# Kernel tuning notes

Hardware: AMD Instinct MI355X
Metric: run time of the kernel (lower is better)

The kernel has to match this reference:

```python
import jax, jax.numpy as jnp
import numpy as np

N = 40000      # nodes
E = 640000     # edges (avg degree 16)
F_IN = 33      # input residue features (hard-coded in module)
H = 128        # hidden_channels
C_OUT = 3      # output classes (hard-coded)
L = 8          # num_layers
ALPHA = 0.1
THETA = 0.5


def setup_inputs() -> dict:
    key = jax.random.key(0)
    ks = jax.random.split(key, 8)
    x = jax.random.normal(ks[0], (N, F_IN), jnp.float32)
    edge_row = jax.random.randint(ks[1], (E,), 0, N)
    edge_col = jax.random.randint(ks[2], (E,), 0, N)
    edge_weight = jax.random.uniform(ks[3], (E,), jnp.float32)
    # nn.Linear stores weight as [out, in]
    W_in = jax.random.normal(ks[4], (H, F_IN), jnp.float32) * 0.1
    b_in = jnp.zeros((H,), jnp.float32)
    W_out = jax.random.normal(ks[5], (C_OUT, H), jnp.float32) * 0.1
    b_out = jnp.zeros((C_OUT,), jnp.float32)
    # GCN2Conv shared weight1 per layer: [L, H, H]
    W_conv = jax.random.normal(ks[6], (L, H, H), jnp.float32) * (1.0 / np.sqrt(H))
    return dict(x=x, edge_row=edge_row, edge_col=edge_col, edge_weight=edge_weight,
                W_in=W_in, b_in=b_in, W_out=W_out, b_out=b_out, W_conv=W_conv)


def reference(x, edge_row, edge_col, edge_weight, W_in, b_in, W_out, b_out, W_conv):
    # dropout p=0.0 -> identity (also eval mode)
    x0 = jax.nn.relu(x @ W_in.T + b_in)                      # [N, H]
    # GCN2Conv beta_l = log(theta / layer + 1), layer = 1..L
    betas = jnp.log(THETA / jnp.arange(1.0, L + 1.0, dtype=jnp.float32) + 1.0)

    def spmm(h):
        # adj_t @ h : gather source-node features, weight, scatter-add to rows
        return jax.ops.segment_sum(edge_weight[:, None] * h[edge_col], edge_row,
                                   num_segments=N)

    def step(xc, lw):
        W, beta = lw
        # GCN2Conv (shared_weights=True, normalize=False):
        #   xx = (1-alpha)*A@h + alpha*x0 ; out = (1-beta)*xx + beta*(xx@W)
        xx = (1.0 - ALPHA) * spmm(xc) + ALPHA * x0
        out = (1.0 - beta) * xx + beta * (xx @ W)
        return xc + jax.nn.relu(out), None                   # residual in GCN.forward

    x_final, _ = jax.lax.scan(step, x0, (W_conv, betas))
    return x_final @ W_out.T + b_out                          # [N, 3]
```

## Files before the change

### kernel.cpp

```cpp
#include <hip/hip_runtime.h>
#include <hip/hip_bf16.h>
#include <math.h>

#define N_NODES 40000
#define NE      640000
#define FIN     33
#define H       128
#define COUT    3
#define NLAYERS 8
#define ALPHA   0.1f
#define THETA   0.5f
#define CAP     96

#define SB_SCAT 625
#define SB_WPRE 512
#define SB_XIN  2500

typedef __bf16 bf16x8 __attribute__((ext_vector_type(8)));
typedef float  f32x4  __attribute__((ext_vector_type(4)));

__device__ inline unsigned short f2bf(float f) {
    __hip_bfloat16 b = __float2bfloat16(f);
    return *(unsigned short*)&b;
}
__device__ inline float bf2f(unsigned short u) {
    __hip_bfloat16 b = *(__hip_bfloat16*)&u;
    return __bfloat162float(b);
}

__global__ __launch_bounds__(256) void k_setup(
        const int* __restrict__ row, const int* __restrict__ col,
        const float* __restrict__ w, int* __restrict__ cnt,
        unsigned int* __restrict__ bucket,
        const float* __restrict__ Wconv, unsigned short* __restrict__ Wtbf,
        const float* __restrict__ x, const float* __restrict__ Win,
        const float* __restrict__ bin,
        unsigned short* __restrict__ x0bf) {
    __shared__ float sW[H * FIN];
    __shared__ float sx[16][FIN];
    int b = blockIdx.x, t = threadIdx.x;

    if (b < SB_SCAT) {
        int e0 = (b * 256 + t) * 4;
        int r[4], pos[4];
        unsigned int rec[4];
        #pragma unroll
        for (int i = 0; i < 4; i++) {
            int e = e0 + i;
            r[i] = row[e];
            unsigned int wb = f2bf((1.0f - ALPHA) * w[e]);
            rec[i] = (wb << 16) | (unsigned int)col[e];
        }
        #pragma unroll
        for (int i = 0; i < 4; i++) pos[i] = atomicAdd(&cnt[r[i]], 1);
        #pragma unroll
        for (int i = 0; i < 4; i++) bucket[(size_t)r[i] * CAP + pos[i]] = rec[i];
        return;
    }
    if (b < SB_SCAT + SB_WPRE) {
        int idx = (b - SB_SCAT) * 256 + t;
        int l = idx >> 14;
        int rem = idx & 16383;
        int k = rem >> 7, j = rem & 127;
        float beta = logf(THETA / (float)(l + 1) + 1.0f);
        float v = beta * Wconv[idx];
        if (j == k) v += 1.0f - beta;
        Wtbf[l * 16384 + j * 128 + k] = f2bf(v);
        return;
    }
    {
        int n0 = (b - SB_SCAT - SB_WPRE) * 16;
        for (int i = t; i < H * FIN; i += 256) sW[i] = Win[i];
        for (int i = t; i < 16 * FIN; i += 256)
            sx[i / FIN][i % FIN] = x[(size_t)(n0 + i / FIN) * FIN + (i % FIN)];
        __syncthreads();
        int f = t % H;
        int l0 = t / H;
        float bv = bin[f];
        for (int lo = l0; lo < 16; lo += 2) {
            float acc = bv;
            #pragma unroll
            for (int k = 0; k < FIN; k++) acc += sx[lo][k] * sW[f * FIN + k];
            acc = fmaxf(acc, 0.f);
            x0bf[(size_t)(n0 + lo) * H + f] = f2bf(acc);
        }
    }
}

__global__ __launch_bounds__(256) void k_layer(
        const int* __restrict__ cnt, const unsigned int* __restrict__ bucket,
        const unsigned short* __restrict__ hin,
        const unsigned short* __restrict__ x0bf,
        const unsigned short* __restrict__ Wt,
        unsigned short* __restrict__ hout,
        const float* __restrict__ Wout, const float* __restrict__ bout,
        float* __restrict__ out, int do_out) {
    __shared__ __align__(16) char smem[16896];

    int t = threadIdx.x;
    int wv = t >> 6, lane = t & 63;
    int rbase = blockIdx.x * 32;

    {
        int slot = lane >> 4;
        int fid  = lane & 15;
        for (int i = 0; i < 8; i++) {
            int rloc = wv * 8 + i;
            int row  = rbase + rloc;
            int deg  = cnt[row];
            const unsigned int* ep = bucket + (size_t)row * CAP;
            float acc[8] = {0,0,0,0,0,0,0,0};

            for (int e = 0; e < deg; e += 16) {
                unsigned int u[4];
                uint4 q[4];
                #pragma unroll
                for (int k = 0; k < 4; k++) {
                    int ei = e + k * 4 + slot;
                    unsigned int uu = ep[ei];
                    u[k] = (ei < deg) ? uu : 0u;
                }
                #pragma unroll
                for (int k = 0; k < 4; k++)
                    q[k] = *(const uint4*)(hin + (size_t)(u[k] & 0xffffu) * H + fid * 8);
                #pragma unroll
                for (int k = 0; k < 4; k++) {
                    float w = bf2f((unsigned short)(u[k] >> 16));
                    acc[0] += w * bf2f((unsigned short)(q[k].x & 0xffffu));
                    acc[1] += w * bf2f((unsigned short)(q[k].x >> 16));
                    acc[2] += w * bf2f((unsigned short)(q[k].y & 0xffffu));
                    acc[3] += w * bf2f((unsigned short)(q[k].y >> 16));
                    acc[4] += w * bf2f((unsigned short)(q[k].z & 0xffffu));
                    acc[5] += w * bf2f((unsigned short)(q[k].z >> 16));
                    acc[6] += w * bf2f((unsigned short)(q[k].w & 0xffffu));
                    acc[7] += w * bf2f((unsigned short)(q[k].w >> 16));
                }
            }
            #pragma unroll
            for (int j = 0; j < 8; j++) {
                acc[j] += __shfl_xor(acc[j], 16);
                acc[j] += __shfl_xor(acc[j], 32);
            }
            if (slot == 0) {
                uint4 xq = *(const uint4*)(x0bf + (size_t)row * H + fid * 8);
                float o0 = acc[0] + ALPHA * bf2f((unsigned short)(xq.x & 0xffffu));
                float o1 = acc[1] + ALPHA * bf2f((unsigned short)(xq.x >> 16));
                float o2 = acc[2] + ALPHA * bf2f((unsigned short)(xq.y & 0xffffu));
                float o3 = acc[3] + ALPHA * bf2f((unsigned short)(xq.y >> 16));
                float o4 = acc[4] + ALPHA * bf2f((unsigned short)(xq.z & 0xffffu));
                float o5 = acc[5] + ALPHA * bf2f((unsigned short)(xq.z >> 16));
                float o6 = acc[6] + ALPHA * bf2f((unsigned short)(xq.w & 0xffffu));
                float o7 = acc[7] + ALPHA * bf2f((unsigned short)(xq.w >> 16));
                uint4 r;
                r.x = (unsigned int)f2bf(o0) | ((unsigned int)f2bf(o1) << 16);
                r.y = (unsigned int)f2bf(o2) | ((unsigned int)f2bf(o3) << 16);
                r.z = (unsigned int)f2bf(o4) | ((unsigned int)f2bf(o5) << 16);
                r.w = (unsigned int)f2bf(o6) | ((unsigned int)f2bf(o7) << 16);
                *(uint4*)(smem + (size_t)rloc * 272 + fid * 16) = r;
            }
        }
    }
    __syncthreads();

    int quad = lane >> 4, l16 = lane & 15;
    int rh = (wv >> 1) * 16;
    int ch = (wv & 1) * 64;
    f32x4 acc2[4];
    #pragma unroll
    for (int j = 0; j < 4; j++) acc2[j] = (f32x4){0.f, 0.f, 0.f, 0.f};

    #pragma unroll
    for (int k0 = 0; k0 < 4; k0++) {
        bf16x8 av = *(const bf16x8*)(smem + (size_t)(rh + l16) * 272 + k0 * 64 + quad * 16);
        #pragma unroll
        for (int j = 0; j < 4; j++) {
            bf16x8 bv = *(const bf16x8*)(Wt + (size_t)(ch + j * 16 + l16) * H + k0 * 32 + quad * 8);
            acc2[j] = __builtin_amdgcn_mfma_f32_16x16x32_bf16(av, bv, acc2[j], 0, 0, 0);
        }
    }
    __syncthreads();

    float* facc = (float*)smem;
    #pragma unroll
    for (int j = 0; j < 4; j++) {
        #pragma unroll
        for (int r = 0; r < 4; r++)
            facc[(rh + quad * 4 + r) * 132 + ch + j * 16 + l16] = acc2[j][r];
    }
    __syncthreads();

    int cb = (t & 15) * 8;
    #pragma unroll
    for (int p = 0; p < 2; p++) {
        int rloc = p * 16 + (t >> 4);
        int row  = rbase + rloc;
        const float* fr = facc + rloc * 132 + cb;
        f32x4 a0 = *(const f32x4*)fr;
        f32x4 a1 = *(const f32x4*)(fr + 4);
        uint4 hq = *(const uint4*)(hin + (size_t)row * H + cb);
        float hv[8];
        hv[0] = bf2f((unsigned short)(hq.x & 0xffffu)) + fmaxf(a0[0], 0.f);
        hv[1] = bf2f((unsigned short)(hq.x >> 16))     + fmaxf(a0[1], 0.f);
        hv[2] = bf2f((unsigned short)(hq.y & 0xffffu)) + fmaxf(a0[2], 0.f);
        hv[3] = bf2f((unsigned short)(hq.y >> 16))     + fmaxf(a0[3], 0.f);
        hv[4] = bf2f((unsigned short)(hq.z & 0xffffu)) + fmaxf(a1[0], 0.f);
        hv[5] = bf2f((unsigned short)(hq.z >> 16))     + fmaxf(a1[1], 0.f);
        hv[6] = bf2f((unsigned short)(hq.w & 0xffffu)) + fmaxf(a1[2], 0.f);
        hv[7] = bf2f((unsigned short)(hq.w >> 16))     + fmaxf(a1[3], 0.f);

        if (!do_out) {
            uint4 rr;
            rr.x = (unsigned int)f2bf(hv[0]) | ((unsigned int)f2bf(hv[1]) << 16);
            rr.y = (unsigned int)f2bf(hv[2]) | ((unsigned int)f2bf(hv[3]) << 16);
            rr.z = (unsigned int)f2bf(hv[4]) | ((unsigned int)f2bf(hv[5]) << 16);
            rr.w = (unsigned int)f2bf(hv[6]) | ((unsigned int)f2bf(hv[7]) << 16);
            *(uint4*)(hout + (size_t)row * H + cb) = rr;
        } else {
            float p0 = 0.f, p1 = 0.f, p2 = 0.f;
            #pragma unroll
            for (int i2 = 0; i2 < 8; i2++) {
                float h = hv[i2];
                p0 += h * Wout[cb + i2];
                p1 += h * Wout[H + cb + i2];
                p2 += h * Wout[2 * H + cb + i2];
            }
            #pragma unroll
            for (int off = 1; off < 16; off <<= 1) {
                p0 += __shfl_xor(p0, off);
                p1 += __shfl_xor(p1, off);
                p2 += __shfl_xor(p2, off);
            }
            if ((t & 15) == 0) {
                out[(size_t)row * 3 + 0] = p0 + bout[0];
                out[(size_t)row * 3 + 1] = p1 + bout[1];
                out[(size_t)row * 3 + 2] = p2 + bout[2];
            }
        }
    }
}

extern "C" void kernel_launch(void* const* d_in, const int* in_sizes, int n_in,
                              void* d_out, int out_size, void* d_ws, size_t ws_size,
                              hipStream_t stream) {
    const float* x     = (const float*)d_in[0];
    const int*   erow  = (const int*)  d_in[1];
    const int*   ecol  = (const int*)  d_in[2];
    const float* ew    = (const float*)d_in[3];
    const float* Win   = (const float*)d_in[4];
    const float* bin   = (const float*)d_in[5];
    const float* Wout  = (const float*)d_in[6];
    const float* bout  = (const float*)d_in[7];
    const float* Wconv = (const float*)d_in[8];
    float* out = (float*)d_out;

    char* ws = (char*)d_ws;
    const size_t NHb = (size_t)N_NODES * H * sizeof(unsigned short);
    unsigned short* x0bf  = (unsigned short*)(ws);
    unsigned short* bufA  = (unsigned short*)(ws + NHb);
    unsigned short* bufB  = (unsigned short*)(ws + 2 * NHb);
    char* p = ws + 3 * NHb;
    unsigned short* Wtbf  = (unsigned short*)p;  p += 8 * H * H * 2;
    int*  cnt     = (int*) p;  p += 160256;
    unsigned int* bucket = (unsigned int*)p;

    hipMemsetAsync(cnt, 0, (size_t)N_NODES * 4, stream);
    k_setup<<<SB_SCAT + SB_WPRE + SB_XIN, 256, 0, stream>>>(
        erow, ecol, ew, cnt, bucket, Wconv, Wtbf, x, Win, bin, x0bf);

    for (int l = 0; l < NLAYERS; l++) {
        const unsigned short* hin = (l == 0) ? x0bf : ((l & 1) ? bufA : bufB);
        unsigned short* hout = (l & 1) ? bufB : bufA;
        k_layer<<<N_NODES / 32, 256, 0, stream>>>(
            cnt, bucket, hin, x0bf, Wtbf + (size_t)l * H * H,
            hout, Wout, bout, out, (l == NLAYERS - 1) ? 1 : 0);
    }
}
```

Baseline: 392.2 us.

## Gather neighbor features as per-row scaled FP8 instead of BF16 in SpMM

Each layer now writes a second copy of the hidden state as FP8 (e4m3) with a per-row max scale, and the sparse aggregation gathers these 128-byte rows plus a scale instead of 256-byte BF16 rows. This halves the random-gather traffic that dominates the SpMM. The residual path keeps a single in-place BF16 buffer. The cost is lower precision in the aggregated features, an extra scale load per edge, a per-row max reduction, and extra FP8 writes per layer.

```diff
diff --git a/kernel.cpp b/kernel.cpp
--- a/kernel.cpp
+++ b/kernel.cpp
@@ -18,6 +18,7 @@
 
 typedef __bf16 bf16x8 __attribute__((ext_vector_type(8)));
 typedef float  f32x4  __attribute__((ext_vector_type(4)));
+typedef float  f32x2  __attribute__((ext_vector_type(2)));
 
 __device__ inline unsigned short f2bf(float f) {
     __hip_bfloat16 b = __float2bfloat16(f);
@@ -35,9 +36,11 @@
         const float* __restrict__ Wconv, unsigned short* __restrict__ Wtbf,
         const float* __restrict__ x, const float* __restrict__ Win,
         const float* __restrict__ bin,
-        unsigned short* __restrict__ x0bf) {
+        unsigned short* __restrict__ x0bf, unsigned char* __restrict__ hf8,
+        float* __restrict__ scl) {
     __shared__ float sW[H * FIN];
     __shared__ float sx[16][FIN];
+    __shared__ int   srm[16];
     int b = blockIdx.x, t = threadIdx.x;
 
     if (b < SB_SCAT) {
@@ -73,26 +76,49 @@
         for (int i = t; i < H * FIN; i += 256) sW[i] = Win[i];
         for (int i = t; i < 16 * FIN; i += 256)
             sx[i / FIN][i % FIN] = x[(size_t)(n0 + i / FIN) * FIN + (i % FIN)];
+        if (t < 16) srm[t] = 0;
         __syncthreads();
         int f = t % H;
         int l0 = t / H;
         float bv = bin[f];
-        for (int lo = l0; lo < 16; lo += 2) {
+        float av[8];
+        #pragma unroll
+        for (int j = 0; j < 8; j++) {
+            int lo = l0 + j * 2;
             float acc = bv;
             #pragma unroll
             for (int k = 0; k < FIN; k++) acc += sx[lo][k] * sW[f * FIN + k];
             acc = fmaxf(acc, 0.f);
+            av[j] = acc;
             x0bf[(size_t)(n0 + lo) * H + f] = f2bf(acc);
+            atomicMax(&srm[lo], __float_as_int(acc));
+        }
+        __syncthreads();
+        #pragma unroll
+        for (int j = 0; j < 8; j++) {
+            int lo = l0 + j * 2;
+            float rm = __int_as_float(srm[lo]);
+            float s448 = rm > 0.f ? 448.f / rm : 0.f;
+            float q  = av[j] * s448;
+            float qn = __shfl_xor(q, 1);
+            if ((f & 1) == 0) {
+                int d = __builtin_amdgcn_cvt_pk_fp8_f32(q, qn, 0, false);
+                *(unsigned short*)(hf8 + (size_t)(n0 + lo) * H + f) =
+                    (unsigned short)(d & 0xffff);
+            }
+            if (f == 0) scl[n0 + lo] = rm * (1.0f / 448.f);
         }
     }
 }
 
 __global__ __launch_bounds__(256) void k_layer(
         const int* __restrict__ cnt, const unsigned int* __restrict__ bucket,
-        const unsigned short* __restrict__ hin,
+        const unsigned char* __restrict__ f8in, const float* __restrict__ scl_in,
+        unsigned char* __restrict__ f8out, float* __restrict__ scl_out,
+        const unsigned short* __restrict__ hres_in,
+        unsigned short* __restrict__ hres_out,
         const unsigned short* __restrict__ x0bf,
         const unsigned short* __restrict__ Wt,
-        unsigned short* __restrict__ hout,
         const float* __restrict__ Wout, const float* __restrict__ bout,
         float* __restrict__ out, int do_out) {
     __shared__ __align__(16) char smem[16896];
@@ -102,61 +128,69 @@
     int rbase = blockIdx.x * 32;
 
     {
-        int slot = lane >> 4;
-        int fid  = lane & 15;
+        int slot = lane >> 3;
+        int fid  = lane & 7;
         for (int i = 0; i < 8; i++) {
             int rloc = wv * 8 + i;
             int row  = rbase + rloc;
             int deg  = cnt[row];
             const unsigned int* ep = bucket + (size_t)row * CAP;
-            float acc[8] = {0,0,0,0,0,0,0,0};
+            float acc[16];
+            #pragma unroll
+            for (int j = 0; j < 16; j++) acc[j] = 0.f;
 
             for (int e = 0; e < deg; e += 16) {
-                unsigned int u[4];
-                uint4 q[4];
-                #pragma unroll
-                for (int k = 0; k < 4; k++) {
-                    int ei = e + k * 4 + slot;
+                unsigned int u[2];
+                float sc[2];
+                uint4 q[2];
+                #pragma unroll
+                for (int k = 0; k < 2; k++) {
+                    int ei = e + k * 8 + slot;
                     unsigned int uu = ep[ei];
                     u[k] = (ei < deg) ? uu : 0u;
                 }
                 #pragma unroll
-                for (int k = 0; k < 4; k++)
-                    q[k] = *(const uint4*)(hin + (size_t)(u[k] & 0xffffu) * H + fid * 8);
-                #pragma unroll
-                for (int k = 0; k < 4; k++) {
-                    float w = bf2f((unsigned short)(u[k] >> 16));
-                    acc[0] += w * bf2f((unsigned short)(q[k].x & 0xffffu));
-                    acc[1] += w * bf2f((unsigned short)(q[k].x >> 16));
-                    acc[2] += w * bf2f((unsigned short)(q[k].y & 0xffffu));
-                    acc[3] += w * bf2f((unsigned short)(q[k].y >> 16));
-                    acc[4] += w * bf2f((unsigned short)(q[k].z & 0xffffu));
-                    acc[5] += w * bf2f((unsigned short)(q[k].z >> 16));
-                    acc[6] += w * bf2f((unsigned short)(q[k].w & 0xffffu));
-                    acc[7] += w * bf2f((unsigned short)(q[k].w >> 16));
+                for (int k = 0; k < 2; k++) sc[k] = scl_in[u[k] & 0xffffu];
+                #pragma unroll
+                for (int k = 0; k < 2; k++)
+                    q[k] = *(const uint4*)(f8in + (size_t)(u[k] & 0xffffu) * H + fid * 16);
+                #pragma unroll
+                for (int k = 0; k < 2; k++) {
+                    float w = bf2f((unsigned short)(u[k] >> 16)) * sc[k];
+                    unsigned int dw[4] = {q[k].x, q[k].y, q[k].z, q[k].w};
+                    #pragma unroll
+                    for (int d = 0; d < 4; d++) {
+                        f32x2 lo = __builtin_amdgcn_cvt_pk_f32_fp8(dw[d], false);
+                        f32x2 hi = __builtin_amdgcn_cvt_pk_f32_fp8(dw[d], true);
+                        acc[d * 4 + 0] += w * lo.x;
+                        acc[d * 4 + 1] += w * lo.y;
+                        acc[d * 4 + 2] += w * hi.x;
+                        acc[d * 4 + 3] += w * hi.y;
+                    }
                 }
             }
             #pragma unroll
-            for (int j = 0; j < 8; j++) {
+            for (int j = 0; j < 16; j++) {
+                acc[j] += __shfl_xor(acc[j], 8);
                 acc[j] += __shfl_xor(acc[j], 16);
                 acc[j] += __shfl_xor(acc[j], 32);
             }
             if (slot == 0) {
-                uint4 xq = *(const uint4*)(x0bf + (size_t)row * H + fid * 8);
-                float o0 = acc[0] + ALPHA * bf2f((unsigned short)(xq.x & 0xffffu));
-                float o1 = acc[1] + ALPHA * bf2f((unsigned short)(xq.x >> 16));
-                float o2 = acc[2] + ALPHA * bf2f((unsigned short)(xq.y & 0xffffu));
-                float o3 = acc[3] + ALPHA * bf2f((unsigned short)(xq.y >> 16));
-                float o4 = acc[4] + ALPHA * bf2f((unsigned short)(xq.z & 0xffffu));
-                float o5 = acc[5] + ALPHA * bf2f((unsigned short)(xq.z >> 16));
-                float o6 = acc[6] + ALPHA * bf2f((unsigned short)(xq.w & 0xffffu));
-                float o7 = acc[7] + ALPHA * bf2f((unsigned short)(xq.w >> 16));
-                uint4 r;
-                r.x = (unsigned int)f2bf(o0) | ((unsigned int)f2bf(o1) << 16);
-                r.y = (unsigned int)f2bf(o2) | ((unsigned int)f2bf(o3) << 16);
-                r.z = (unsigned int)f2bf(o4) | ((unsigned int)f2bf(o5) << 16);
-                r.w = (unsigned int)f2bf(o6) | ((unsigned int)f2bf(o7) << 16);
-                *(uint4*)(smem + (size_t)rloc * 272 + fid * 16) = r;
+                uint4 xa = *(const uint4*)(x0bf + (size_t)row * H + fid * 16);
+                uint4 xb = *(const uint4*)(x0bf + (size_t)row * H + fid * 16 + 8);
+                unsigned int xw[8] = {xa.x, xa.y, xa.z, xa.w, xb.x, xb.y, xb.z, xb.w};
+                uint4 r0, r1;
+                unsigned int rr[8];
+                #pragma unroll
+                for (int p = 0; p < 8; p++) {
+                    float o0 = acc[p * 2 + 0] + ALPHA * bf2f((unsigned short)(xw[p] & 0xffffu));
+                    float o1 = acc[p * 2 + 1] + ALPHA * bf2f((unsigned short)(xw[p] >> 16));
+                    rr[p] = (unsigned int)f2bf(o0) | ((unsigned int)f2bf(o1) << 16);
+                }
+                r0.x = rr[0]; r0.y = rr[1]; r0.z = rr[2]; r0.w = rr[3];
+                r1.x = rr[4]; r1.y = rr[5]; r1.z = rr[6]; r1.w = rr[7];
+                *(uint4*)(smem + (size_t)rloc * 272 + fid * 32) = r0;
+                *(uint4*)(smem + (size_t)rloc * 272 + fid * 32 + 16) = r1;
             }
         }
     }
@@ -197,7 +231,7 @@
         const float* fr = facc + rloc * 132 + cb;
         f32x4 a0 = *(const f32x4*)fr;
         f32x4 a1 = *(const f32x4*)(fr + 4);
-        uint4 hq = *(const uint4*)(hin + (size_t)row * H + cb);
+        uint4 hq = *(const uint4*)(hres_in + (size_t)row * H + cb);
         float hv[8];
         hv[0] = bf2f((unsigned short)(hq.x & 0xffffu)) + fmaxf(a0[0], 0.f);
         hv[1] = bf2f((unsigned short)(hq.x >> 16))     + fmaxf(a0[1], 0.f);
@@ -214,7 +248,21 @@
             rr.y = (unsigned int)f2bf(hv[2]) | ((unsigned int)f2bf(hv[3]) << 16);
             rr.z = (unsigned int)f2bf(hv[4]) | ((unsigned int)f2bf(hv[5]) << 16);
             rr.w = (unsigned int)f2bf(hv[6]) | ((unsigned int)f2bf(hv[7]) << 16);
-            *(uint4*)(hout + (size_t)row * H + cb) = rr;
+            *(uint4*)(hres_out + (size_t)row * H + cb) = rr;
+            float rm = hv[0];
+            #pragma unroll
+            for (int j = 1; j < 8; j++) rm = fmaxf(rm, hv[j]);
+            #pragma unroll
+            for (int off = 1; off < 16; off <<= 1)
+                rm = fmaxf(rm, __shfl_xor(rm, off));
+            float s448 = rm > 0.f ? 448.f / rm : 0.f;
+            int d0 = __builtin_amdgcn_cvt_pk_fp8_f32(hv[0] * s448, hv[1] * s448, 0, false);
+            d0     = __builtin_amdgcn_cvt_pk_fp8_f32(hv[2] * s448, hv[3] * s448, d0, true);
+            int d1 = __builtin_amdgcn_cvt_pk_fp8_f32(hv[4] * s448, hv[5] * s448, 0, false);
+            d1     = __builtin_amdgcn_cvt_pk_fp8_f32(hv[6] * s448, hv[7] * s448, d1, true);
+            uint2 f8v; f8v.x = (unsigned int)d0; f8v.y = (unsigned int)d1;
+            *(uint2*)(f8out + (size_t)row * H + cb) = f8v;
+            if ((t & 15) == 0) scl_out[row] = rm * (1.0f / 448.f);
         } else {
             float p0 = 0.f, p1 = 0.f, p2 = 0.f;
             #pragma unroll
@@ -255,23 +303,31 @@
 
     char* ws = (char*)d_ws;
     const size_t NHb = (size_t)N_NODES * H * sizeof(unsigned short);
-    unsigned short* x0bf  = (unsigned short*)(ws);
-    unsigned short* bufA  = (unsigned short*)(ws + NHb);
-    unsigned short* bufB  = (unsigned short*)(ws + 2 * NHb);
-    char* p = ws + 3 * NHb;
-    unsigned short* Wtbf  = (unsigned short*)p;  p += 8 * H * H * 2;
-    int*  cnt     = (int*) p;  p += 160256;
+    const size_t NH8 = (size_t)N_NODES * H;
+    unsigned short* x0bf = (unsigned short*)(ws);
+    unsigned short* hbf  = (unsigned short*)(ws + NHb);
+    unsigned char*  hf8A = (unsigned char*)(ws + 2 * NHb);
+    unsigned char*  hf8B = (unsigned char*)(ws + 2 * NHb + NH8);
+    char* p = ws + 2 * NHb + 2 * NH8;
+    unsigned short* Wtbf = (unsigned short*)p;  p += 8 * H * H * 2;
+    int*   cnt  = (int*)  p;  p += 160256;
+    float* sclA = (float*)p;  p += 160256;
+    float* sclB = (float*)p;  p += 160256;
     unsigned int* bucket = (unsigned int*)p;
 
     hipMemsetAsync(cnt, 0, (size_t)N_NODES * 4, stream);
     k_setup<<<SB_SCAT + SB_WPRE + SB_XIN, 256, 0, stream>>>(
-        erow, ecol, ew, cnt, bucket, Wconv, Wtbf, x, Win, bin, x0bf);
+        erow, ecol, ew, cnt, bucket, Wconv, Wtbf, x, Win, bin, x0bf, hf8A, sclA);
 
     for (int l = 0; l < NLAYERS; l++) {
-        const unsigned short* hin = (l == 0) ? x0bf : ((l & 1) ? bufA : bufB);
-        unsigned short* hout = (l & 1) ? bufB : bufA;
+        const unsigned char* f8in  = (l & 1) ? hf8B : hf8A;
+        unsigned char*       f8out = (l & 1) ? hf8A : hf8B;
+        const float* scl_in  = (l & 1) ? sclB : sclA;
+        float*       scl_out = (l & 1) ? sclA : sclB;
+        const unsigned short* hres_in = (l == 0) ? x0bf : hbf;
         k_layer<<<N_NODES / 32, 256, 0, stream>>>(
-            cnt, bucket, hin, x0bf, Wtbf + (size_t)l * H * H,
-            hout, Wout, bout, out, (l == NLAYERS - 1) ? 1 : 0);
-    }
-}
+            cnt, bucket, f8in, scl_in, f8out, scl_out, hres_in, hbf, x0bf,
+            Wtbf + (size_t)l * H * H, Wout, bout, out,
+            (l == NLAYERS - 1) ? 1 : 0);
+    }
+}
```

Result: slower. 456.9 us (+16.5%).

## Gather neighbor features in scaled FP8 instead of BF16 for layers after the first

Applied to the files above, without the earlier changes.

Each layer's output is now also stored as FP8 (e4m3), scaled by a global running max that is tracked with atomicMax. The next layer's sparse aggregation gathers these 1-byte values and dequantizes them with the matching scale. This halves the bytes moved by the random neighbor gathers, which dominate the cost. The residual path keeps a single in-place BF16 buffer. The quantization scale for a layer's output comes from the previous layer's max with a fixed headroom of 16, so values can clip or lose precision, which puts accuracy tolerance at risk.

```diff
diff --git a/kernel.cpp b/kernel.cpp
--- a/kernel.cpp
+++ b/kernel.cpp
@@ -11,6 +11,7 @@
 #define ALPHA   0.1f
 #define THETA   0.5f
 #define CAP     96
+#define HEADROOM 16.0f
 
 #define SB_SCAT 625
 #define SB_WPRE 512
@@ -18,6 +19,7 @@
 
 typedef __bf16 bf16x8 __attribute__((ext_vector_type(8)));
 typedef float  f32x4  __attribute__((ext_vector_type(4)));
+typedef float  f32x2  __attribute__((ext_vector_type(2)));
 
 __device__ inline unsigned short f2bf(float f) {
     __hip_bfloat16 b = __float2bfloat16(f);
@@ -35,7 +37,7 @@
         const float* __restrict__ Wconv, unsigned short* __restrict__ Wtbf,
         const float* __restrict__ x, const float* __restrict__ Win,
         const float* __restrict__ bin,
-        unsigned short* __restrict__ x0bf) {
+        unsigned short* __restrict__ x0bf, int* __restrict__ gmaxb) {
     __shared__ float sW[H * FIN];
     __shared__ float sx[16][FIN];
     int b = blockIdx.x, t = threadIdx.x;
@@ -77,24 +79,28 @@
         int f = t % H;
         int l0 = t / H;
         float bv = bin[f];
+        float tmax = 0.f;
         for (int lo = l0; lo < 16; lo += 2) {
             float acc = bv;
             #pragma unroll
             for (int k = 0; k < FIN; k++) acc += sx[lo][k] * sW[f * FIN + k];
             acc = fmaxf(acc, 0.f);
+            tmax = fmaxf(tmax, acc);
             x0bf[(size_t)(n0 + lo) * H + f] = f2bf(acc);
         }
-    }
-}
-
-__global__ __launch_bounds__(256) void k_layer(
+        #pragma unroll
+        for (int off = 1; off < 64; off <<= 1)
+            tmax = fmaxf(tmax, __shfl_xor(tmax, off));
+        if ((t & 63) == 0) atomicMax(&gmaxb[0], __float_as_int(tmax));
+    }
+}
+
+__global__ __launch_bounds__(256) void k_layer0(
         const int* __restrict__ cnt, const unsigned int* __restrict__ bucket,
-        const unsigned short* __restrict__ hin,
         const unsigned short* __restrict__ x0bf,
         const unsigned short* __restrict__ Wt,
-        unsigned short* __restrict__ hout,
-        const float* __restrict__ Wout, const float* __restrict__ bout,
-        float* __restrict__ out, int do_out) {
+        unsigned short* __restrict__ hbf,
+        unsigned char* __restrict__ f8out, int* __restrict__ gmaxb) {
     __shared__ __align__(16) char smem[16896];
 
     int t = threadIdx.x;
@@ -122,7 +128,7 @@
                 }
                 #pragma unroll
                 for (int k = 0; k < 4; k++)
-                    q[k] = *(const uint4*)(hin + (size_t)(u[k] & 0xffffu) * H + fid * 8);
+                    q[k] = *(const uint4*)(x0bf + (size_t)(u[k] & 0xffffu) * H + fid * 8);
                 #pragma unroll
                 for (int k = 0; k < 4; k++) {
                     float w = bf2f((unsigned short)(u[k] >> 16));
@@ -168,7 +174,6 @@
     f32x4 acc2[4];
     #pragma unroll
     for (int j = 0; j < 4; j++) acc2[j] = (f32x4){0.f, 0.f, 0.f, 0.f};
-
     #pragma unroll
     for (int k0 = 0; k0 < 4; k0++) {
         bf16x8 av = *(const bf16x8*)(smem + (size_t)(rh + l16) * 272 + k0 * 64 + quad * 16);
@@ -189,7 +194,10 @@
     }
     __syncthreads();
 
+    float g0 = __int_as_float(gmaxb[0]);
+    float Q = g0 > 0.f ? 448.f / (HEADROOM * g0) : 0.f;
     int cb = (t & 15) * 8;
+    float rmax = 0.f;
     #pragma unroll
     for (int p = 0; p < 2; p++) {
         int rloc = p * 16 + (t >> 4);
@@ -197,7 +205,7 @@
         const float* fr = facc + rloc * 132 + cb;
         f32x4 a0 = *(const f32x4*)fr;
         f32x4 a1 = *(const f32x4*)(fr + 4);
-        uint4 hq = *(const uint4*)(hin + (size_t)row * H + cb);
+        uint4 hq = *(const uint4*)(x0bf + (size_t)row * H + cb);
         float hv[8];
         hv[0] = bf2f((unsigned short)(hq.x & 0xffffu)) + fmaxf(a0[0], 0.f);
         hv[1] = bf2f((unsigned short)(hq.x >> 16))     + fmaxf(a0[1], 0.f);
@@ -208,13 +216,177 @@
         hv[6] = bf2f((unsigned short)(hq.w & 0xffffu)) + fmaxf(a1[2], 0.f);
         hv[7] = bf2f((unsigned short)(hq.w >> 16))     + fmaxf(a1[3], 0.f);
 
+        uint4 rr;
+        rr.x = (unsigned int)f2bf(hv[0]) | ((unsigned int)f2bf(hv[1]) << 16);
+        rr.y = (unsigned int)f2bf(hv[2]) | ((unsigned int)f2bf(hv[3]) << 16);
+        rr.z = (unsigned int)f2bf(hv[4]) | ((unsigned int)f2bf(hv[5]) << 16);
+        rr.w = (unsigned int)f2bf(hv[6]) | ((unsigned int)f2bf(hv[7]) << 16);
+        *(uint4*)(hbf + (size_t)row * H + cb) = rr;
+
+        int d0 = __builtin_amdgcn_cvt_pk_fp8_f32(hv[0] * Q, hv[1] * Q, 0, false);
+        d0     = __builtin_amdgcn_cvt_pk_fp8_f32(hv[2] * Q, hv[3] * Q, d0, true);
+        int d1 = __builtin_amdgcn_cvt_pk_fp8_f32(hv[4] * Q, hv[5] * Q, 0, false);
+        d1     = __builtin_amdgcn_cvt_pk_fp8_f32(hv[6] * Q, hv[7] * Q, d1, true);
+        uint2 f8v; f8v.x = (unsigned int)d0; f8v.y = (unsigned int)d1;
+        *(uint2*)(f8out + (size_t)row * H + cb) = f8v;
+
+        #pragma unroll
+        for (int j = 0; j < 8; j++) rmax = fmaxf(rmax, hv[j]);
+    }
+    #pragma unroll
+    for (int off = 1; off < 64; off <<= 1)
+        rmax = fmaxf(rmax, __shfl_xor(rmax, off));
+    if ((t & 63) == 0) atomicMax(&gmaxb[1], __float_as_int(rmax));
+}
+
+__global__ __launch_bounds__(256) void k_layerf8(
+        const int* __restrict__ cnt, const unsigned int* __restrict__ bucket,
+        const unsigned char* __restrict__ f8in,
+        unsigned char* __restrict__ f8out,
+        unsigned short* __restrict__ hbf,
+        const unsigned short* __restrict__ x0bf,
+        const unsigned short* __restrict__ Wt,
+        int* __restrict__ gmaxb, int li,
+        const float* __restrict__ Wout, const float* __restrict__ bout,
+        float* __restrict__ out, int do_out) {
+    __shared__ __align__(16) char smem[16896];
+
+    int t = threadIdx.x;
+    int wv = t >> 6, lane = t & 63;
+    int rbase = blockIdx.x * 32;
+
+    float gin = __int_as_float(gmaxb[li - 1]);
+    float D = gin > 0.f ? (HEADROOM / 448.f) * gin : 0.f;
+
+    {
+        int slot = lane >> 3;
+        int fid  = lane & 7;
+        for (int i = 0; i < 8; i++) {
+            int rloc = wv * 8 + i;
+            int row  = rbase + rloc;
+            int deg  = cnt[row];
+            const unsigned int* ep = bucket + (size_t)row * CAP;
+            float acc[16];
+            #pragma unroll
+            for (int j = 0; j < 16; j++) acc[j] = 0.f;
+
+            for (int e = 0; e < deg; e += 16) {
+                unsigned int u[2];
+                uint4 q[2];
+                #pragma unroll
+                for (int k = 0; k < 2; k++) {
+                    int ei = e + k * 8 + slot;
+                    unsigned int uu = ep[ei];
+                    u[k] = (ei < deg) ? uu : 0u;
+                }
+                #pragma unroll
+                for (int k = 0; k < 2; k++)
+                    q[k] = *(const uint4*)(f8in + (size_t)(u[k] & 0xffffu) * H + fid * 16);
+                #pragma unroll
+                for (int k = 0; k < 2; k++) {
+                    float w = bf2f((unsigned short)(u[k] >> 16));
+                    unsigned int dw[4] = {q[k].x, q[k].y, q[k].z, q[k].w};
+                    #pragma unroll
+                    for (int d = 0; d < 4; d++) {
+                        f32x2 lo = __builtin_amdgcn_cvt_pk_f32_fp8(dw[d], false);
+                        f32x2 hi = __builtin_amdgcn_cvt_pk_f32_fp8(dw[d], true);
+                        acc[d * 4 + 0] += w * lo.x;
+                        acc[d * 4 + 1] += w * lo.y;
+                        acc[d * 4 + 2] += w * hi.x;
+                        acc[d * 4 + 3] += w * hi.y;
+                    }
+                }
+            }
+            #pragma unroll
+            for (int j = 0; j < 16; j++) {
+                acc[j] += __shfl_xor(acc[j], 8);
+                acc[j] += __shfl_xor(acc[j], 16);
+                acc[j] += __shfl_xor(acc[j], 32);
+            }
+            if (slot == 0) {
+                uint4 xa = *(const uint4*)(x0bf + (size_t)row * H + fid * 16);
+                uint4 xb = *(const uint4*)(x0bf + (size_t)row * H + fid * 16 + 8);
+                unsigned int xw[8] = {xa.x, xa.y, xa.z, xa.w, xb.x, xb.y, xb.z, xb.w};
+                uint4 r0, r1;
+                unsigned int rr[8];
+                #pragma unroll
+                for (int p = 0; p < 8; p++) {
+                    float o0 = acc[p * 2 + 0] * D + ALPHA * bf2f((unsigned short)(xw[p] & 0xffffu));
+                    float o1 = acc[p * 2 + 1] * D + ALPHA * bf2f((unsigned short)(xw[p] >> 16));
+                    rr[p] = (unsigned int)f2bf(o0) | ((unsigned int)f2bf(o1) << 16);
+                }
+                r0.x = rr[0]; r0.y = rr[1]; r0.z = rr[2]; r0.w = rr[3];
+                r1.x = rr[4]; r1.y = rr[5]; r1.z = rr[6]; r1.w = rr[7];
+                *(uint4*)(smem + (size_t)rloc * 272 + fid * 32) = r0;
+                *(uint4*)(smem + (size_t)rloc * 272 + fid * 32 + 16) = r1;
+            }
+        }
+    }
+    __syncthreads();
+
+    int quad = lane >> 4, l16 = lane & 15;
+    int rh = (wv >> 1) * 16;
+    int ch = (wv & 1) * 64;
+    f32x4 acc2[4];
+    #pragma unroll
+    for (int j = 0; j < 4; j++) acc2[j] = (f32x4){0.f, 0.f, 0.f, 0.f};
+    #pragma unroll
+    for (int k0 = 0; k0 < 4; k0++) {
+        bf16x8 av = *(const bf16x8*)(smem + (size_t)(rh + l16) * 272 + k0 * 64 + quad * 16);
+        #pragma unroll
+        for (int j = 0; j < 4; j++) {
+            bf16x8 bv = *(const bf16x8*)(Wt + (size_t)(ch + j * 16 + l16) * H + k0 * 32 + quad * 8);
+            acc2[j] = __builtin_amdgcn_mfma_f32_16x16x32_bf16(av, bv, acc2[j], 0, 0, 0);
+        }
+    }
+    __syncthreads();
+
+    float* facc = (float*)smem;
+    #pragma unroll
+    for (int j = 0; j < 4; j++) {
+        #pragma unroll
+        for (int r = 0; r < 4; r++)
+            facc[(rh + quad * 4 + r) * 132 + ch + j * 16 + l16] = acc2[j][r];
+    }
+    __syncthreads();
+
+    float gq = __int_as_float(gmaxb[li]);
+    float Q = gq > 0.f ? 448.f / (HEADROOM * gq) : 0.f;
+    int cb = (t & 15) * 8;
+    float rmax = 0.f;
+    #pragma unroll
+    for (int p = 0; p < 2; p++) {
+        int rloc = p * 16 + (t >> 4);
+        int row  = rbase + rloc;
+        const float* fr = facc + rloc * 132 + cb;
+        f32x4 a0 = *(const f32x4*)fr;
+        f32x4 a1 = *(const f32x4*)(fr + 4);
+        uint4 hq = *(const uint4*)(hbf + (size_t)row * H + cb);
+        float hv[8];
+        hv[0] = bf2f((unsigned short)(hq.x & 0xffffu)) + fmaxf(a0[0], 0.f);
+        hv[1] = bf2f((unsigned short)(hq.x >> 16))     + fmaxf(a0[1], 0.f);
+        hv[2] = bf2f((unsigned short)(hq.y & 0xffffu)) + fmaxf(a0[2], 0.f);
+        hv[3] = bf2f((unsigned short)(hq.y >> 16))     + fmaxf(a0[3], 0.f);
+        hv[4] = bf2f((unsigned short)(hq.z & 0xffffu)) + fmaxf(a1[0], 0.f);
+        hv[5] = bf2f((unsigned short)(hq.z >> 16))     + fmaxf(a1[1], 0.f);
+        hv[6] = bf2f((unsigned short)(hq.w & 0xffffu)) + fmaxf(a1[2], 0.f);
+        hv[7] = bf2f((unsigned short)(hq.w >> 16))     + fmaxf(a1[3], 0.f);
+
         if (!do_out) {
             uint4 rr;
             rr.x = (unsigned int)f2bf(hv[0]) | ((unsigned int)f2bf(hv[1]) << 16);
             rr.y = (unsigned int)f2bf(hv[2]) | ((unsigned int)f2bf(hv[3]) << 16);
             rr.z = (unsigned int)f2bf(hv[4]) | ((unsigned int)f2bf(hv[5]) << 16);
             rr.w = (unsigned int)f2bf(hv[6]) | ((unsigned int)f2bf(hv[7]) << 16);
-            *(uint4*)(hout + (size_t)row * H + cb) = rr;
+            *(uint4*)(hbf + (size_t)row * H + cb) = rr;
+            int d0 = __builtin_amdgcn_cvt_pk_fp8_f32(hv[0] * Q, hv[1] * Q, 0, false);
+            d0     = __builtin_amdgcn_cvt_pk_fp8_f32(hv[2] * Q, hv[3] * Q, d0, true);
+            int d1 = __builtin_amdgcn_cvt_pk_fp8_f32(hv[4] * Q, hv[5] * Q, 0, false);
+            d1     = __builtin_amdgcn_cvt_pk_fp8_f32(hv[6] * Q, hv[7] * Q, d1, true);
+            uint2 f8v; f8v.x = (unsigned int)d0; f8v.y = (unsigned int)d1;
+            *(uint2*)(f8out + (size_t)row * H + cb) = f8v;
+            #pragma unroll
+            for (int j = 0; j < 8; j++) rmax = fmaxf(rmax, hv[j]);
         } else {
             float p0 = 0.f, p1 = 0.f, p2 = 0.f;
             #pragma unroll
@@ -236,6 +408,12 @@
                 out[(size_t)row * 3 + 2] = p2 + bout[2];
             }
         }
+    }
+    if (!do_out) {
+        #pragma unroll
+        for (int off = 1; off < 64; off <<= 1)
+            rmax = fmaxf(rmax, __shfl_xor(rmax, off));
+        if ((t & 63) == 0) atomicMax(&gmaxb[li + 1], __float_as_int(rmax));
     }
 }
 
@@ -255,23 +433,31 @@
 
     char* ws = (char*)d_ws;
     const size_t NHb = (size_t)N_NODES * H * sizeof(unsigned short);
-    unsigned short* x0bf  = (unsigned short*)(ws);
-    unsigned short* bufA  = (unsigned short*)(ws + NHb);
-    unsigned short* bufB  = (unsigned short*)(ws + 2 * NHb);
-    char* p = ws + 3 * NHb;
-    unsigned short* Wtbf  = (unsigned short*)p;  p += 8 * H * H * 2;
-    int*  cnt     = (int*) p;  p += 160256;
+    const size_t NH8 = (size_t)N_NODES * H;
+    unsigned short* x0bf = (unsigned short*)(ws);
+    unsigned short* hbf  = (unsigned short*)(ws + NHb);
+    unsigned char*  hf8A = (unsigned char*)(ws + 2 * NHb);
+    unsigned char*  hf8B = (unsigned char*)(ws + 2 * NHb + NH8);
+    char* p = ws + 2 * NHb + 2 * NH8;
+    unsigned short* Wtbf = (unsigned short*)p;  p += 8 * H * H * 2;
+    int* cnt   = (int*)p;
+    int* gmaxb = (int*)(p + 160000);
+    p += 160256;
     unsigned int* bucket = (unsigned int*)p;
 
-    hipMemsetAsync(cnt, 0, (size_t)N_NODES * 4, stream);
+    hipMemsetAsync(cnt, 0, 160256, stream);
     k_setup<<<SB_SCAT + SB_WPRE + SB_XIN, 256, 0, stream>>>(
-        erow, ecol, ew, cnt, bucket, Wconv, Wtbf, x, Win, bin, x0bf);
-
-    for (int l = 0; l < NLAYERS; l++) {
-        const unsigned short* hin = (l == 0) ? x0bf : ((l & 1) ? bufA : bufB);
-        unsigned short* hout = (l & 1) ? bufB : bufA;
-        k_layer<<<N_NODES / 32, 256, 0, stream>>>(
-            cnt, bucket, hin, x0bf, Wtbf + (size_t)l * H * H,
-            hout, Wout, bout, out, (l == NLAYERS - 1) ? 1 : 0);
-    }
-}
+        erow, ecol, ew, cnt, bucket, Wconv, Wtbf, x, Win, bin, x0bf, gmaxb);
+
+    k_layer0<<<N_NODES / 32, 256, 0, stream>>>(
+        cnt, bucket, x0bf, Wtbf, hbf, hf8A, gmaxb);
+
+    for (int l = 1; l < NLAYERS; l++) {
+        const unsigned char* f8in  = ((l - 1) & 1) ? hf8B : hf8A;
+        unsigned char*       f8out = ((l - 1) & 1) ? hf8A : hf8B;
+        k_layerf8<<<N_NODES / 32, 256, 0, stream>>>(
+            cnt, bucket, f8in, f8out, hbf, x0bf,
+            Wtbf + (size_t)l * H * H, gmaxb, l, Wout, bout, out,
+            (l == NLAYERS - 1) ? 1 : 0);
+    }
+}
```

Result: slower. 902.3 us (+130.0%).
